# Kernel optimization log

Hardware: AMD Instinct MI355X
Metric: run time of the kernel (lower is better)

## Reference

```python
import jax, jax.numpy as jnp
import numpy as np
from jax import lax

KSIZE = 5
NKER = 16
UNITS = 10


def _clean(x):
    return jnp.where(jnp.isnan(x) | jnp.isinf(x), jnp.zeros_like(x), x)


def setup_inputs() -> dict:
    key = jax.random.key(0)
    k1, k2, k3 = jax.random.split(key, 3)
    x = jax.random.normal(k1, (16, 1, 28, 28), dtype=jnp.float32)
    conv_w_mu = 0.05 * jax.random.normal(k2, (NKER, 1, KSIZE, KSIZE), dtype=jnp.float32)
    conv_w_sigma = jnp.full((NKER,), -2.2, dtype=jnp.float32)
    fc_w_mu = 0.05 * jax.random.normal(k3, (2304, UNITS), dtype=jnp.float32)
    fc_w_sigma = jnp.full((UNITS,), -2.2, dtype=jnp.float32)
    return {"x": x, "conv_w_mu": conv_w_mu, "conv_w_sigma": conv_w_sigma,
            "fc_w_mu": fc_w_mu, "fc_w_sigma": fc_w_sigma}


def _forward(x, conv_w_mu, conv_w_sigma, fc_w_mu, fc_w_sigma):
    B = x.shape[0]
    # ---- VDPFirstConv ----
    mu1 = lax.conv_general_dilated(x, conv_w_mu, (1, 1), 'VALID',
                                   dimension_numbers=('NCHW', 'OIHW', 'NCHW'))  # [B,K,24,24]
    # patches ordered (c, kh, kw) in feature dim, matching torch unfold+permute
    patches = lax.conv_general_dilated_patches(x, (KSIZE, KSIZE), (1, 1), 'VALID')  # [B,25,24,24]
    P = patches.shape[-1] * patches.shape[-2]  # 576
    xm = patches.reshape(B, patches.shape[1], P).transpose(0, 2, 1)  # [B,576,25]
    xxt = jnp.einsum('bpk,bqk->bpq', xm, xm)  # [B,576,576]
    sp1 = jnp.log1p(jnp.exp(conv_w_sigma))  # softplus, [K]
    sigma1 = sp1[None, :, None, None] * xxt[:, None, :, :]  # [B,K,576,576]
    sigma1 = _clean(sigma1)
    # ---- VDPReLU ----
    mu2 = jax.nn.relu(mu1)
    g = (mu1 > 0).astype(mu1.dtype).reshape(B, NKER, -1)  # [B,K,576]
    sigma2 = sigma1 * (g[..., :, None] * g[..., None, :])
    # ---- VDPMaxPooling (2x2, stride 2) ----
    H = mu2.shape[-1]
    Ho = H // 2
    win = mu2.reshape(B, NKER, Ho, 2, Ho, 2).transpose(0, 1, 2, 4, 3, 5).reshape(B, NKER, Ho, Ho, 4)
    mu3 = win.max(axis=-1)  # [B,K,12,12]
    a = jnp.argmax(win, axis=-1)  # [B,K,12,12]
    ii = jnp.arange(Ho)[:, None]
    jj = jnp.arange(Ho)[None, :]
    h = 2 * ii + a // 2
    w = 2 * jj + a % 2
    idx = (h * H + w).reshape(B, NKER, Ho * Ho)  # flat index into 576, [B,K,144]
    s = jnp.take_along_axis(sigma2, idx[:, :, :, None], axis=2)  # [B,K,144,576]
    sigma3 = jnp.take_along_axis(s, idx[:, :, None, :], axis=3)  # [B,K,144,144]
    # ---- VDPFlattenAndFC ----
    mu_flatt = mu3.reshape(B, -1)  # [B,2304], (K,h,w) order
    mu4 = mu_flatt @ fc_w_mu  # [B,units]
    fcw = fc_w_mu.reshape(NKER, Ho * Ho, UNITS)  # [K,144,U]
    sigma_a = jnp.einsum('kiu,bkij,kjv->buv', fcw, sigma3, fcw)  # [B,U,U]
    tr = jnp.trace(sigma3, axis1=2, axis2=3).sum(axis=1, keepdims=True)  # [B,1]
    sp2 = jnp.log1p(jnp.exp(fc_w_sigma))  # [U]
    eye = jnp.eye(UNITS, dtype=mu4.dtype)
    sigma_b = (sp2 * tr)[:, :, None] * eye  # diag_embed
    mnorm = jnp.sum(mu_flatt * mu_flatt, axis=1, keepdims=True)  # [B,1]
    sigma_c = (sp2 * mnorm)[:, :, None] * eye
    sigma4 = _clean(sigma_a + sigma_b + sigma_c)
    # ---- MySoftmax ----
    p = jax.nn.softmax(mu4, axis=-1)
    grad = p[:, :, None] * eye - p[:, :, None] * p[:, None, :]  # diag(p) - p p^T
    sigma_out = jnp.einsum('bij,bjk,blk->bil', grad, sigma4, grad)
    sigma_out = _clean(sigma_out)
    sigma_out = _clean(sigma_out)
    return p, sigma_out


def reference(x, conv_w_mu, conv_w_sigma, fc_w_mu, fc_w_sigma):
    return _forward(x, conv_w_mu, conv_w_sigma, fc_w_mu, fc_w_sigma)
```

## Files before the change

### kernel.cpp

```cpp
#include <hip/hip_runtime.h>
#include <math.h>

#define BATCH 16
#define NKER  16
#define KS    5
#define UNITS 10
#define HIN   28
#define HOUT  24
#define PO    12
#define NPOOL (PO*PO)
#define NC    (KS*KS)
#define PCOLS 26
#define PART  112

__global__ __launch_bounds__(256) void vdp_stage1(
    const float* __restrict__ x,
    const float* __restrict__ conv_w,
    const float* __restrict__ conv_s,
    const float* __restrict__ fc_w,
    float* __restrict__ ws)
{
    const int bk = blockIdx.x;
    const int b  = bk >> 4;
    const int k  = bk & 15;
    const int t  = threadIdx.x;

    __shared__ float xs[HIN*HIN];
    __shared__ float cw[NC];
    __shared__ float fcw_s[NPOOL*UNITS];
    __shared__ float P_s[NPOOL*PCOLS];
    __shared__ float T_s[UNITS*PCOLS];
    __shared__ float red_s[4][12];
    __shared__ float fin_s[12];
    __shared__ float sp1s;

    {
        const float4* x4 = reinterpret_cast<const float4*>(x + b*HIN*HIN);
        float4* xs4 = reinterpret_cast<float4*>(xs);
        for (int i = t; i < HIN*HIN/4; i += 256) xs4[i] = x4[i];
        const float4* f4 = reinterpret_cast<const float4*>(fc_w + k*NPOOL*UNITS);
        float4* fs4 = reinterpret_cast<float4*>(fcw_s);
        for (int i = t; i < NPOOL*UNITS/4; i += 256) fs4[i] = f4[i];
        if (t < NC) cw[t] = conv_w[k*NC + t];
        if (t == 0) sp1s = log1pf(expf(conv_s[k]));
    }
    __syncthreads();

    float v_tr = 0.f, v_mn = 0.f;
    float v_mu[UNITS];
    #pragma unroll
    for (int u = 0; u < UNITS; ++u) v_mu[u] = 0.f;

    if (t < NPOOL) {
        const int pi = t / PO, pj = t - pi*PO;
        float w6[36];
        #pragma unroll
        for (int r = 0; r < 6; ++r)
            #pragma unroll
            for (int cc = 0; cc < 6; ++cc)
                w6[r*6 + cc] = xs[(2*pi + r)*HIN + 2*pj + cc];
        float cwr[NC];
        #pragma unroll
        for (int c = 0; c < NC; ++c) cwr[c] = cw[c];

        float a0 = 0.f, a1 = 0.f, a2 = 0.f, a3 = 0.f;
        #pragma unroll
        for (int kh = 0; kh < KS; ++kh)
            #pragma unroll
            for (int kw = 0; kw < KS; ++kw) {
                const float w = cwr[kh*KS + kw];
                a0 = fmaf(w, w6[kh*6 + kw],       a0);
                a1 = fmaf(w, w6[kh*6 + kw + 1],   a1);
                a2 = fmaf(w, w6[(kh+1)*6 + kw],   a2);
                a3 = fmaf(w, w6[(kh+1)*6 + kw+1], a3);
            }
        const float r0 = fmaxf(a0, 0.f), r1 = fmaxf(a1, 0.f);
        const float r2 = fmaxf(a2, 0.f), r3 = fmaxf(a3, 0.f);
        float bestv = r0; int besta = 0;
        if (r1 > bestv) { bestv = r1; besta = 1; }
        if (r2 > bestv) { bestv = r2; besta = 2; }
        if (r3 > bestv) { bestv = r3; besta = 3; }
        const float mu3 = bestv;
        const float g   = (mu3 > 0.f) ? 1.f : 0.f;

        float ns = 0.f;
        #pragma unroll
        for (int kh = 0; kh < KS; ++kh)
            #pragma unroll
            for (int kw = 0; kw < KS; ++kw) {
                const float v0 = w6[kh*6 + kw];
                const float v1 = w6[kh*6 + kw + 1];
                const float v2 = w6[(kh+1)*6 + kw];
                const float v3 = w6[(kh+1)*6 + kw + 1];
                const float val = (besta < 2) ? ((besta == 0) ? v0 : v1)
                                              : ((besta == 2) ? v2 : v3);
                const float pv = g * val;
                P_s[t*PCOLS + kh*KS + kw] = pv;
                ns = fmaf(pv, pv, ns);
            }
        P_s[t*PCOLS + NC] = 0.f;
        v_tr = ns;
        v_mn = mu3*mu3;
        #pragma unroll
        for (int u = 0; u < UNITS; ++u) v_mu[u] = mu3*fcw_s[t*UNITS + u];
    }

    {
        float vals[12];
        vals[0] = v_tr; vals[1] = v_mn;
        #pragma unroll
        for (int u = 0; u < UNITS; ++u) vals[2+u] = v_mu[u];
        #pragma unroll
        for (int off = 32; off >= 1; off >>= 1)
            #pragma unroll
            for (int j = 0; j < 12; ++j)
                vals[j] += __shfl_down(vals[j], off);
        const int wid = t >> 6, lane = t & 63;
        if (lane == 0)
            #pragma unroll
            for (int j = 0; j < 12; ++j) red_s[wid][j] = vals[j];
    }
    __syncthreads();
    if (t < 12) fin_s[t] = red_s[0][t] + red_s[1][t] + red_s[2][t] + red_s[3][t];

    if (t < UNITS*13) {
        const int u = t / 13, j = t - u*13;
        const int c0 = 2*j;
        float acc0 = 0.f, acc1 = 0.f;
        #pragma unroll 8
        for (int i = 0; i < NPOOL; ++i) {
            const float w = fcw_s[i*UNITS + u];
            const float2 pv = *reinterpret_cast<const float2*>(&P_s[i*PCOLS + c0]);
            acc0 = fmaf(w, pv.x, acc0);
            acc1 = fmaf(w, pv.y, acc1);
        }
        T_s[u*PCOLS + c0]     = acc0;
        T_s[u*PCOLS + c0 + 1] = acc1;
    }
    __syncthreads();

    float* wsp = ws + bk*PART;
    if (t < UNITS*UNITS) {
        const int u = t / UNITS, v = t - u*UNITS;
        float s = 0.f;
        #pragma unroll
        for (int c = 0; c < NC; ++c) s = fmaf(T_s[u*PCOLS + c], T_s[v*PCOLS + c], s);
        wsp[t] = sp1s * s;
    } else if (t < UNITS*UNITS + UNITS) {
        wsp[t] = fin_s[2 + (t - UNITS*UNITS)];
    } else if (t == PART - 2) {
        wsp[PART-2] = sp1s * fin_s[0];
    } else if (t == PART - 1) {
        wsp[PART-1] = fin_s[1];
    }
}

__global__ __launch_bounds__(128) void vdp_stage2(
    const float* __restrict__ ws,
    const float* __restrict__ fc_s,
    float* __restrict__ out)
{
    const int b = blockIdx.x;
    const int t = threadIdx.x;

    __shared__ float s[PART];
    __shared__ float s4[UNITS*UNITS];
    __shared__ float tmp[UNITS*UNITS];
    __shared__ float p_s[UNITS];
    __shared__ float r_s[UNITS];
    __shared__ float q_s[UNITS];
    __shared__ float sp2[UNITS];

    if (t < PART) {
        float a = 0.f;
        #pragma unroll
        for (int k = 0; k < NKER; ++k) a += ws[(b*NKER + k)*PART + t];
        s[t] = a;
    }
    if (t < UNITS) sp2[t] = log1pf(expf(fc_s[t]));
    __syncthreads();

    if (t < UNITS*UNITS) {
        const int u = t / UNITS, v = t - u*UNITS;
        float a = s[t];
        if (u == v) a += sp2[u]*(s[PART-2] + s[PART-1]);
        s4[t] = a;
    }
    if (t == 112) {
        float mx = s[100];
        #pragma unroll
        for (int u = 1; u < UNITS; ++u) mx = fmaxf(mx, s[100+u]);
        float sum = 0.f;
        float e[UNITS];
        #pragma unroll
        for (int u = 0; u < UNITS; ++u) { e[u] = expf(s[100+u] - mx); sum += e[u]; }
        #pragma unroll
        for (int u = 0; u < UNITS; ++u) p_s[u] = e[u] / sum;
    }
    __syncthreads();

    if (t < UNITS) {
        float r = 0.f;
        #pragma unroll
        for (int j = 0; j < UNITS; ++j) r = fmaf(p_s[j], s4[j*UNITS + t], r);
        r_s[t] = r;
    }
    __syncthreads();
    if (t < UNITS*UNITS) {
        const int i = t / UNITS, k2 = t - i*UNITS;
        tmp[t] = p_s[i]*(s4[t] - r_s[k2]);
    }
    __syncthreads();
    if (t < UNITS) {
        float q = 0.f;
        #pragma unroll
        for (int k = 0; k < UNITS; ++k) q = fmaf(tmp[t*UNITS + k], p_s[k], q);
        q_s[t] = q;
    }
    __syncthreads();
    if (t < UNITS*UNITS) {
        const int i = t / UNITS, l = t - i*UNITS;
        out[BATCH*UNITS + b*UNITS*UNITS + t] = p_s[l]*(tmp[i*UNITS + l] - q_s[i]);
    }
    if (t < UNITS) out[b*UNITS + t] = p_s[t];
}

extern "C" void kernel_launch(void* const* d_in, const int* in_sizes, int n_in,
                              void* d_out, int out_size, void* d_ws, size_t ws_size,
                              hipStream_t stream) {
    const float* x      = (const float*)d_in[0];
    const float* conv_w = (const float*)d_in[1];
    const float* conv_s = (const float*)d_in[2];
    const float* fc_w   = (const float*)d_in[3];
    const float* fc_s   = (const float*)d_in[4];
    float* out = (float*)d_out;
    float* ws  = (float*)d_ws;

    vdp_stage1<<<BATCH*NKER, 256, 0, stream>>>(x, conv_w, conv_s, fc_w, ws);
    vdp_stage2<<<BATCH, 128, 0, stream>>>(ws, fc_s, out);
}
```

Baseline: 14.48 us.

## Fuse both stages into one per-batch kernel with gathered patch GEMM

Merges the per-(batch,kernel) stage and the per-batch reduction stage into a single 1024-thread block per batch element. This removes the second launch and the workspace round trip. Instead of materialising the masked patch matrix in shared memory, it stores a gather index per pooled cell that points at a zero pad when the ReLU is inactive. The fc weights times patch product is then computed with register tiles and a shuffle reduction, reading fc_w straight from global memory. The cost is only 16 blocks on the GPU, so parallelism is much lower, and each thread carries heavier register state.

```diff
diff --git a/kernel.cpp b/kernel.cpp
--- a/kernel.cpp
+++ b/kernel.cpp
@@ -10,39 +10,43 @@
 #define PO    12
 #define NPOOL (PO*PO)
 #define NC    (KS*KS)
-#define PCOLS 26
-#define PART  112
-
-__global__ __launch_bounds__(256) void vdp_stage1(
+#define NCELL (NKER*NPOOL)
+#define XSZ   928
+#define TPAD  28
+
+__global__ __launch_bounds__(1024) void vdp_one(
     const float* __restrict__ x,
     const float* __restrict__ conv_w,
     const float* __restrict__ conv_s,
     const float* __restrict__ fc_w,
-    float* __restrict__ ws)
+    const float* __restrict__ fc_s,
+    float* __restrict__ out)
 {
-    const int bk = blockIdx.x;
-    const int b  = bk >> 4;
-    const int k  = bk & 15;
-    const int t  = threadIdx.x;
-
-    __shared__ float xs[HIN*HIN];
-    __shared__ float cw[NC];
-    __shared__ float fcw_s[NPOOL*UNITS];
-    __shared__ float P_s[NPOOL*PCOLS];
-    __shared__ float T_s[UNITS*PCOLS];
-    __shared__ float red_s[4][12];
+    const int b = blockIdx.x;
+    const int t = threadIdx.x;
+
+    __shared__ float xs[XSZ];
+    __shared__ float cw[NKER*NC];
+    __shared__ float sp1[NKER];
+    __shared__ float sp2[UNITS];
+    __shared__ short idx_s[NCELL];
+    __shared__ float T_s[NKER][UNITS][TPAD];
+    __shared__ float A_s[NKER][UNITS*UNITS];
+    __shared__ float red_s[16][12];
     __shared__ float fin_s[12];
-    __shared__ float sp1s;
+    __shared__ float s_[UNITS*UNITS];
+    __shared__ float s4[UNITS*UNITS];
+    __shared__ float tmp[UNITS*UNITS];
+    __shared__ float p_s[UNITS], r_s[UNITS], q_s[UNITS];
 
     {
         const float4* x4 = reinterpret_cast<const float4*>(x + b*HIN*HIN);
         float4* xs4 = reinterpret_cast<float4*>(xs);
-        for (int i = t; i < HIN*HIN/4; i += 256) xs4[i] = x4[i];
-        const float4* f4 = reinterpret_cast<const float4*>(fc_w + k*NPOOL*UNITS);
-        float4* fs4 = reinterpret_cast<float4*>(fcw_s);
-        for (int i = t; i < NPOOL*UNITS/4; i += 256) fs4[i] = f4[i];
-        if (t < NC) cw[t] = conv_w[k*NC + t];
-        if (t == 0) sp1s = log1pf(expf(conv_s[k]));
+        if (t < HIN*HIN/4) xs4[t] = x4[t];
+        if (t >= 784 && t < XSZ) xs[t] = 0.f;
+        if (t >= 512 && t < 512 + NKER*NC) cw[t-512] = conv_w[t-512];
+        if (t < NKER) sp1[t] = log1pf(expf(conv_s[t]));
+        if (t >= 32 && t < 32 + UNITS) sp2[t-32] = log1pf(expf(fc_s[t-32]));
     }
     __syncthreads();
 
@@ -51,24 +55,23 @@
     #pragma unroll
     for (int u = 0; u < UNITS; ++u) v_mu[u] = 0.f;
 
-    if (t < NPOOL) {
-        const int pi = t / PO, pj = t - pi*PO;
+    for (int cell = t; cell < NCELL; cell += 1024) {
+        const int k  = cell / NPOOL;
+        const int m  = cell - k*NPOOL;
+        const int pi = m / PO, pj = m - pi*PO;
         float w6[36];
         #pragma unroll
         for (int r = 0; r < 6; ++r)
             #pragma unroll
             for (int cc = 0; cc < 6; ++cc)
                 w6[r*6 + cc] = xs[(2*pi + r)*HIN + 2*pj + cc];
-        float cwr[NC];
-        #pragma unroll
-        for (int c = 0; c < NC; ++c) cwr[c] = cw[c];
 
         float a0 = 0.f, a1 = 0.f, a2 = 0.f, a3 = 0.f;
         #pragma unroll
         for (int kh = 0; kh < KS; ++kh)
             #pragma unroll
             for (int kw = 0; kw < KS; ++kw) {
-                const float w = cwr[kh*KS + kw];
+                const float w = cw[k*NC + kh*KS + kw];
                 a0 = fmaf(w, w6[kh*6 + kw],       a0);
                 a1 = fmaf(w, w6[kh*6 + kw + 1],   a1);
                 a2 = fmaf(w, w6[(kh+1)*6 + kw],   a2);
@@ -94,15 +97,17 @@
                 const float v3 = w6[(kh+1)*6 + kw + 1];
                 const float val = (besta < 2) ? ((besta == 0) ? v0 : v1)
                                               : ((besta == 2) ? v2 : v3);
-                const float pv = g * val;
-                P_s[t*PCOLS + kh*KS + kw] = pv;
-                ns = fmaf(pv, pv, ns);
+                ns = fmaf(val, val, ns);
             }
-        P_s[t*PCOLS + NC] = 0.f;
-        v_tr = ns;
-        v_mn = mu3*mu3;
-        #pragma unroll
-        for (int u = 0; u < UNITS; ++u) v_mu[u] = mu3*fcw_s[t*UNITS + u];
+        const int oh = 2*pi + (besta >> 1);
+        const int ow = 2*pj + (besta & 1);
+        idx_s[cell] = (short)((g > 0.f) ? (oh*HIN + ow) : 784);
+
+        v_tr = fmaf(g*sp1[k], ns, v_tr);
+        v_mn = fmaf(mu3, mu3, v_mn);
+        const float* fr = fc_w + cell*UNITS;
+        #pragma unroll
+        for (int u = 0; u < UNITS; ++u) v_mu[u] = fmaf(mu3, fr[u], v_mu[u]);
     }
 
     {
@@ -121,84 +126,100 @@
             for (int j = 0; j < 12; ++j) red_s[wid][j] = vals[j];
     }
     __syncthreads();
-    if (t < 12) fin_s[t] = red_s[0][t] + red_s[1][t] + red_s[2][t] + red_s[3][t];
-
-    if (t < UNITS*13) {
-        const int u = t / 13, j = t - u*13;
-        const int c0 = 2*j;
-        float acc0 = 0.f, acc1 = 0.f;
-        #pragma unroll 8
-        for (int i = 0; i < NPOOL; ++i) {
-            const float w = fcw_s[i*UNITS + u];
-            const float2 pv = *reinterpret_cast<const float2*>(&P_s[i*PCOLS + c0]);
-            acc0 = fmaf(w, pv.x, acc0);
-            acc1 = fmaf(w, pv.y, acc1);
+    if (t < 12) {
+        float a = 0.f;
+        #pragma unroll
+        for (int w = 0; w < 16; ++w) a += red_s[w][t];
+        fin_s[t] = a;
+    }
+
+    {
+        const int k  = t >> 6;
+        const int ln = t & 63;
+        const int iq = ln & 7;
+        const int ch = (ln >> 3) & 3;
+        const int uh = ln >> 5;
+        const int u0 = uh*5;
+        const int c0 = ch*7;
+        int off_c[7];
+        #pragma unroll
+        for (int cc = 0; cc < 7; ++cc) {
+            const int c = c0 + cc;
+            const int kh = c / KS, kw = c - kh*KS;
+            off_c[cc] = kh*HIN + kw;
         }
-        T_s[u*PCOLS + c0]     = acc0;
-        T_s[u*PCOLS + c0 + 1] = acc1;
-    }
-    __syncthreads();
-
-    float* wsp = ws + bk*PART;
-    if (t < UNITS*UNITS) {
-        const int u = t / UNITS, v = t - u*UNITS;
+        float acc[5][7];
+        #pragma unroll
+        for (int uu = 0; uu < 5; ++uu)
+            #pragma unroll
+            for (int cc = 0; cc < 7; ++cc) acc[uu][cc] = 0.f;
+
+        const int ibase = k*NPOOL + iq*18;
+        #pragma unroll 3
+        for (int ii = 0; ii < 18; ++ii) {
+            const int base = idx_s[ibase + ii];
+            const float* wp = fc_w + (ibase + ii)*UNITS + u0;
+            float wv[5];
+            #pragma unroll
+            for (int uu = 0; uu < 5; ++uu) wv[uu] = wp[uu];
+            float pv[7];
+            #pragma unroll
+            for (int cc = 0; cc < 7; ++cc) pv[cc] = xs[base + off_c[cc]];
+            #pragma unroll
+            for (int uu = 0; uu < 5; ++uu)
+                #pragma unroll
+                for (int cc = 0; cc < 7; ++cc)
+                    acc[uu][cc] = fmaf(wv[uu], pv[cc], acc[uu][cc]);
+        }
+        #pragma unroll
+        for (int off = 4; off >= 1; off >>= 1)
+            #pragma unroll
+            for (int uu = 0; uu < 5; ++uu)
+                #pragma unroll
+                for (int cc = 0; cc < 7; ++cc)
+                    acc[uu][cc] += __shfl_down(acc[uu][cc], off, 8);
+        if (iq == 0)
+            #pragma unroll
+            for (int uu = 0; uu < 5; ++uu)
+                #pragma unroll
+                for (int cc = 0; cc < 7; ++cc)
+                    T_s[k][u0+uu][c0+cc] = acc[uu][cc];
+    }
+    __syncthreads();
+
+    for (int task = t; task < NKER*UNITS*UNITS; task += 1024) {
+        const int k2 = task / (UNITS*UNITS);
+        const int uv = task - k2*(UNITS*UNITS);
+        const int u = uv / UNITS, v = uv - u*UNITS;
         float s = 0.f;
         #pragma unroll
-        for (int c = 0; c < NC; ++c) s = fmaf(T_s[u*PCOLS + c], T_s[v*PCOLS + c], s);
-        wsp[t] = sp1s * s;
-    } else if (t < UNITS*UNITS + UNITS) {
-        wsp[t] = fin_s[2 + (t - UNITS*UNITS)];
-    } else if (t == PART - 2) {
-        wsp[PART-2] = sp1s * fin_s[0];
-    } else if (t == PART - 1) {
-        wsp[PART-1] = fin_s[1];
-    }
-}
-
-__global__ __launch_bounds__(128) void vdp_stage2(
-    const float* __restrict__ ws,
-    const float* __restrict__ fc_s,
-    float* __restrict__ out)
-{
-    const int b = blockIdx.x;
-    const int t = threadIdx.x;
-
-    __shared__ float s[PART];
-    __shared__ float s4[UNITS*UNITS];
-    __shared__ float tmp[UNITS*UNITS];
-    __shared__ float p_s[UNITS];
-    __shared__ float r_s[UNITS];
-    __shared__ float q_s[UNITS];
-    __shared__ float sp2[UNITS];
-
-    if (t < PART) {
-        float a = 0.f;
-        #pragma unroll
-        for (int k = 0; k < NKER; ++k) a += ws[(b*NKER + k)*PART + t];
-        s[t] = a;
-    }
-    if (t < UNITS) sp2[t] = log1pf(expf(fc_s[t]));
-    __syncthreads();
-
-    if (t < UNITS*UNITS) {
-        const int u = t / UNITS, v = t - u*UNITS;
-        float a = s[t];
-        if (u == v) a += sp2[u]*(s[PART-2] + s[PART-1]);
-        s4[t] = a;
-    }
-    if (t == 112) {
-        float mx = s[100];
-        #pragma unroll
-        for (int u = 1; u < UNITS; ++u) mx = fmaxf(mx, s[100+u]);
+        for (int c = 0; c < NC; ++c) s = fmaf(T_s[k2][u][c], T_s[k2][v][c], s);
+        A_s[k2][uv] = sp1[k2]*s;
+    }
+    if (t == 1023) {
+        float mx = fin_s[2];
+        #pragma unroll
+        for (int u = 1; u < UNITS; ++u) mx = fmaxf(mx, fin_s[2+u]);
         float sum = 0.f;
         float e[UNITS];
         #pragma unroll
-        for (int u = 0; u < UNITS; ++u) { e[u] = expf(s[100+u] - mx); sum += e[u]; }
+        for (int u = 0; u < UNITS; ++u) { e[u] = expf(fin_s[2+u] - mx); sum += e[u]; }
         #pragma unroll
         for (int u = 0; u < UNITS; ++u) p_s[u] = e[u] / sum;
     }
     __syncthreads();
 
+    if (t < UNITS*UNITS) {
+        float a = 0.f;
+        #pragma unroll
+        for (int k = 0; k < NKER; ++k) a += A_s[k][t];
+        s_[t] = a;
+        const int u = t / UNITS, v = t - u*UNITS;
+        float s4v = a;
+        if (u == v) s4v += sp2[u]*(fin_s[0] + fin_s[1]);
+        s4[t] = s4v;
+    }
+    __syncthreads();
     if (t < UNITS) {
         float r = 0.f;
         #pragma unroll
@@ -214,7 +235,7 @@
     if (t < UNITS) {
         float q = 0.f;
         #pragma unroll
-        for (int k = 0; k < UNITS; ++k) q = fmaf(tmp[t*UNITS + k], p_s[k], q);
+        for (int kk = 0; kk < UNITS; ++kk) q = fmaf(tmp[t*UNITS + kk], p_s[kk], q);
         q_s[t] = q;
     }
     __syncthreads();
@@ -234,8 +255,5 @@
     const float* fc_w   = (const float*)d_in[3];
     const float* fc_s   = (const float*)d_in[4];
     float* out = (float*)d_out;
-    float* ws  = (float*)d_ws;
-
-    vdp_stage1<<<BATCH*NKER, 256, 0, stream>>>(x, conv_w, conv_s, fc_w, ws);
-    vdp_stage2<<<BATCH, 128, 0, stream>>>(ws, fc_s, out);
+    vdp_one<<<BATCH, 1024, 0, stream>>>(x, conv_w, conv_s, fc_w, fc_s, out);
 }
```

Result: slower. 27.90 us (+92.7%).
